# Performance work log

Hardware: AMD Instinct MI355X
Metric: run time of the kernel (lower is better)

The kernel has to match this reference:

```python
import jax, jax.numpy as jnp
import numpy as np

HIDDEN = 1280
NUM_HEADS = 16
HEAD_DIM = HIDDEN // NUM_HEADS  # 80
ROPE_DIM = HEAD_DIM // 2        # 40
THETA = 10000.0
SEQ = 3072


def setup_inputs() -> dict:
    key = jax.random.key(0)
    ks = jax.random.split(key, 6)
    hidden_states = jax.random.normal(ks[0], (SEQ, HIDDEN), dtype=jnp.float32)
    position_ids = jax.random.randint(ks[1], (SEQ, 2), 0, 64, dtype=jnp.int32)
    qkv_w = jax.random.normal(ks[2], (HIDDEN, 3 * HIDDEN), dtype=jnp.float32) * (HIDDEN ** -0.5)
    qkv_b = jax.random.normal(ks[3], (3 * HIDDEN,), dtype=jnp.float32) * 0.02
    o_w = jax.random.normal(ks[4], (HIDDEN, HIDDEN), dtype=jnp.float32) * (HIDDEN ** -0.5)
    o_b = jax.random.normal(ks[5], (HIDDEN,), dtype=jnp.float32) * 0.02
    return {"hidden_states": hidden_states, "position_ids": position_ids,
            "qkv_w": qkv_w, "qkv_b": qkv_b, "o_w": o_w, "o_b": o_b}


def _rotate_half(x):
    x1, x2 = jnp.split(x, 2, axis=-1)
    return jnp.concatenate([-x2, x1], axis=-1)


def reference(hidden_states, position_ids, qkv_w, qkv_b, o_w, o_b):
    seq_len = hidden_states.shape[0]
    # fused QKV projection
    qkv = hidden_states @ qkv_w + qkv_b                     # (S, 3*H*D)
    qkv = qkv.reshape(seq_len, 3, NUM_HEADS, HEAD_DIM)
    q, k, v = qkv[:, 0], qkv[:, 1], qkv[:, 2]               # each (S, h, d)
    # 2D RoPE: inv_freq over rope dim = head_dim // 2
    inv_freq = 1.0 / (THETA ** (jnp.arange(0, ROPE_DIM, 2, dtype=jnp.float32) / ROPE_DIM))
    pos = position_ids.astype(jnp.float32)
    h_freqs = jnp.outer(pos[:, 0], inv_freq)                # (S, rope/2)
    w_freqs = jnp.outer(pos[:, 1], inv_freq)                # (S, rope/2)
    freqs = jnp.concatenate([h_freqs, w_freqs], axis=-1)    # (S, rope)
    emb = jnp.concatenate([freqs, freqs], axis=-1)          # (S, head_dim)
    cos = jnp.cos(emb)[:, None, :]                          # (S, 1, d)
    sin = jnp.sin(emb)[:, None, :]
    q = q * cos + _rotate_half(q) * sin
    k = k * cos + _rotate_half(k) * sin
    # manual attention
    scaling = HEAD_DIM ** -0.5
    attn = jnp.einsum('qhd,khd->hqk', q * scaling, k)       # (h, S, S)
    attn = jax.nn.softmax(attn, axis=-1)
    out = jnp.einsum('hqk,khd->qhd', attn, v)               # (S, h, d)
    out = out.reshape(seq_len, HIDDEN)
    return out @ o_w + o_b
```

## Files before the change

### kernel.cpp

```cpp
#include <hip/hip_runtime.h>

#define SEQ  3072
#define HID  1280
#define NH   16
#define HD   80
#define NQKV 3840
#define KSP  2

typedef unsigned short u16;
typedef unsigned int u32;
typedef __attribute__((ext_vector_type(8))) short short8;
typedef __attribute__((ext_vector_type(4))) short short4v;
typedef __attribute__((ext_vector_type(4))) float floatx4;

__device__ __forceinline__ u16 f2bf(float x) {
    u32 u = __float_as_uint(x);
    u += 0x7fffu + ((u >> 16) & 1u);
    return (u16)(u >> 16);
}
__device__ __forceinline__ u32 packrne(float a, float b) {
    return (u32)f2bf(a) | ((u32)f2bf(b) << 16);
}

typedef const __attribute__((address_space(1))) unsigned int* gp1_t;
typedef __attribute__((address_space(3))) unsigned int* lp3_t;
__device__ __forceinline__ void gld16(const void* g, void* l) {
    __builtin_amdgcn_global_load_lds((gp1_t)g, (lp3_t)l, 16, 0, 0);
}

__device__ __forceinline__ int swz80(int c, int r) {
    return (c < 8) ? (c ^ (r & 7)) : (8 + ((c - 8) ^ ((r >> 2) & 1)));
}

__global__ void prep_k(const int* __restrict__ pos, float* __restrict__ cosb,
                       float* __restrict__ sinb, const float* __restrict__ hs,
                       u16* __restrict__ hH, const float* __restrict__ qkvw,
                       u16* __restrict__ wT, const float* __restrict__ ow,
                       u16* __restrict__ owT) {
    __shared__ float tile[32][33];
    const int b = blockIdx.x, t = threadIdx.x;
    if (b < 480) {
        int i = b * 256 + t;
        int s = i / 40, j = i % 40;
        float p = (float)((j < 20) ? pos[s * 2] : pos[s * 2 + 1]);
        int k = (j < 20) ? j : j - 20;
        float inv = powf(10000.0f, -(float)k / 20.0f);
        float a = p * inv;
        cosb[s * 40 + j] = cosf(a);
        sinb[s * 40 + j] = sinf(a);
    } else if (b < 4320) {
        int i = (b - 480) * 256 + t;
        const float4 x = ((const float4*)hs)[i];
        uint2 o;
        o.x = packrne(x.x, x.y);
        o.y = packrne(x.z, x.w);
        ((uint2*)hH)[i] = o;
    } else {
        const float* w;
        u16* dst;
        int K, N, nx, ky;
        if (b < 9120) {
            int i = b - 4320;
            nx = i % 120; ky = i / 120; w = qkvw; dst = wT; K = HID; N = NQKV;
        } else {
            int i = b - 9120;
            nx = i % 40; ky = i / 40; w = ow; dst = owT; K = HID; N = HID;
        }
        int n0 = nx * 32, k0 = ky * 32;
        int c = t & 31, r8 = t >> 5;
        for (int rr = r8; rr < 32; rr += 8)
            tile[rr][c] = w[(size_t)(k0 + rr) * N + n0 + c];
        __syncthreads();
        for (int rr = r8; rr < 32; rr += 8)
            dst[(size_t)(n0 + rr) * K + k0 + c] = f2bf(tile[c][rr]);
    }
}

__global__ __launch_bounds__(256, 3) void gemm_bf16_k(
    const u16* __restrict__ A, const u16* __restrict__ B,
    const float* __restrict__ bias, float* __restrict__ C,
    int M, int N, int K, int mode) {
    __shared__ u16 lA[128 * 64], lB[128 * 64];
    const int t = threadIdx.x, lane = t & 63, w = t >> 6;
    const int qi = lane & 15, quad = lane >> 4;
    int id = blockIdx.x;
    int xcd = id & 7, sN = id >> 3;
    int m_idx, n_idx;
    if (mode == 0) {
        n_idx = (xcd & 1) * 15 + sN % 15;
        m_idx = (xcd >> 1) * 6 + sN / 15;
    } else {
        m_idx = xcd * 3 + sN / 10;
        n_idx = sN % 10;
    }
    const int m0 = m_idx * 128, n0 = n_idx * 128;
    const int wm = (w >> 1) * 64, wn = (w & 1) * 64;

    floatx4 acc[4][4];
    for (int mi = 0; mi < 4; mi++)
        for (int ni = 0; ni < 4; ni++) acc[mi][ni] = (floatx4){0.f, 0.f, 0.f, 0.f};

    const int rg = lane >> 3;
    const int ce = ((lane & 7) ^ rg) * 8;
    size_t gA[4], gB[4];
    for (int g = 0; g < 4; g++) {
        int row = w * 32 + g * 8 + rg;
        gA[g] = (size_t)(m0 + row) * K + ce;
        gB[g] = (size_t)(n0 + row) * K + ce;
    }

    for (int k0 = 0; k0 < K; k0 += 64) {
        for (int g = 0; g < 4; g++) {
            gld16(A + gA[g] + k0, &lA[(w * 32 + g * 8) * 64]);
            gld16(B + gB[g] + k0, &lB[(w * 32 + g * 8) * 64]);
        }
        __syncthreads();
        short8 af[4][2], bf[4][2];
        for (int mi = 0; mi < 4; mi++) {
            int row = wm + mi * 16 + qi;
            for (int kh = 0; kh < 2; kh++)
                af[mi][kh] = *(const short8*)&lA[row * 64 + (((kh * 4 + quad) ^ (row & 7)) << 3)];
        }
        for (int ni = 0; ni < 4; ni++) {
            int row = wn + ni * 16 + qi;
            for (int kh = 0; kh < 2; kh++)
                bf[ni][kh] = *(const short8*)&lB[row * 64 + (((kh * 4 + quad) ^ (row & 7)) << 3)];
        }
        for (int mi = 0; mi < 4; mi++)
            for (int ni = 0; ni < 4; ni++) {
                acc[mi][ni] = __builtin_amdgcn_mfma_f32_16x16x32_bf16(af[mi][0], bf[ni][0], acc[mi][ni], 0, 0, 0);
                acc[mi][ni] = __builtin_amdgcn_mfma_f32_16x16x32_bf16(af[mi][1], bf[ni][1], acc[mi][ni], 0, 0, 0);
            }
        __syncthreads();
    }
    for (int mi = 0; mi < 4; mi++)
        for (int ni = 0; ni < 4; ni++) {
            int col = n0 + wn + ni * 16 + qi;
            int rowb = m0 + wm + mi * 16 + quad * 4;
            float b = bias[col];
            for (int r = 0; r < 4; r++)
                C[(size_t)(rowb + r) * N + col] = acc[mi][ni][r] + b;
        }
}

__global__ void pack_qkv_k(const float* __restrict__ qkv, const float* __restrict__ cosb,
                           const float* __restrict__ sinb,
                           u16* __restrict__ Qs, u16* __restrict__ Ks, u16* __restrict__ Vs) {
    __shared__ float lv[80 * 65];
    const int t = threadIdx.x;
    const int h = blockIdx.y, s0 = blockIdx.x * 64;
    const float qsc = 0.11180339887498949f * 1.4426950408889634f;

    for (int i = t; i < 64 * 10; i += 256) {
        int rl = i / 10, jg = i % 10;
        int s = s0 + rl, j = jg * 4;
        const float4 cc = *(const float4*)&cosb[s * 40 + j];
        const float4 ss = *(const float4*)&sinb[s * 40 + j];
        const float* qb = qkv + (size_t)s * NQKV + h * HD;
        const float4 q1 = *(const float4*)&qb[j];
        const float4 q2 = *(const float4*)&qb[j + 40];
        const float* kb = qb + HID;
        const float4 k1 = *(const float4*)&kb[j];
        const float4 k2 = *(const float4*)&kb[j + 40];
        uint2 qo1, qo2, ko1, ko2;
        qo1.x = packrne((q1.x * cc.x - q2.x * ss.x) * qsc, (q1.y * cc.y - q2.y * ss.y) * qsc);
        qo1.y = packrne((q1.z * cc.z - q2.z * ss.z) * qsc, (q1.w * cc.w - q2.w * ss.w) * qsc);
        qo2.x = packrne((q2.x * cc.x + q1.x * ss.x) * qsc, (q2.y * cc.y + q1.y * ss.y) * qsc);
        qo2.y = packrne((q2.z * cc.z + q1.z * ss.z) * qsc, (q2.w * cc.w + q1.w * ss.w) * qsc);
        ko1.x = packrne(k1.x * cc.x - k2.x * ss.x, k1.y * cc.y - k2.y * ss.y);
        ko1.y = packrne(k1.z * cc.z - k2.z * ss.z, k1.w * cc.w - k2.w * ss.w);
        ko2.x = packrne(k2.x * cc.x + k1.x * ss.x, k2.y * cc.y + k1.y * ss.y);
        ko2.y = packrne(k2.z * cc.z + k1.z * ss.z, k2.w * cc.w + k1.w * ss.w);
        size_t base = (size_t)(h * SEQ + s) * 80;
        int sub0 = j & 7, sub1 = (j + 40) & 7;
        int p0 = swz80(j >> 3, s);
        int p1 = swz80((j + 40) >> 3, s);
        *(uint2*)&Qs[base + p0 * 8 + sub0] = qo1;
        *(uint2*)&Qs[base + p1 * 8 + sub1] = qo2;
        *(uint2*)&Ks[base + p0 * 8 + sub0] = ko1;
        *(uint2*)&Ks[base + p1 * 8 + sub1] = ko2;
    }
    for (int i = t; i < 64 * 80; i += 256) {
        int rl = i / 80, d = i % 80;
        lv[d * 65 + rl] = qkv[(size_t)(s0 + rl) * NQKV + 2 * HID + h * HD + d];
    }
    __syncthreads();
    for (int i = t; i < 80 * 16; i += 256) {
        int d = i / 16, g = i % 16;
        int c2l = g * 4;
        float v0 = lv[d * 65 + c2l], v1 = lv[d * 65 + c2l + 1];
        float v2 = lv[d * 65 + c2l + 2], v3 = lv[d * 65 + c2l + 3];
        int pc = (g >> 1) ^ (d & 7);
        uint2 o;
        o.x = packrne(v0, v1);
        o.y = packrne(v2, v3);
        *(uint2*)&Vs[((size_t)h * HD + d) * SEQ + s0 + pc * 8 + (g & 1) * 4] = o;
    }
}

__global__ __launch_bounds__(256, 3) void attn_k(
    const u16* __restrict__ Qs, const u16* __restrict__ Ks, const u16* __restrict__ Vs,
    float* __restrict__ Op, float* __restrict__ lp) {
    __shared__ u16 kbuf[2][5120];
    __shared__ u16 vbuf[2][5120];
    __shared__ u16 pls[4][1024];

    const int t = threadIdx.x, lane = t & 63, w = t >> 6;
    const int qi = lane & 15, quad = lane >> 4;
    const int h = blockIdx.y, q0 = blockIdx.x * 128, ksp = blockIdx.z;
    const int kc0 = ksp * (SEQ / 2);
    u16* const kflat = &kbuf[0][0];

    {
        const u16* Qt = Qs + (size_t)(h * SEQ + q0) * 80;
        for (int j = 0; j < 5; j++) {
            int o = (w * 5 + j) * 512;
            gld16(Qt + o + lane * 8, kflat + o);
        }
    }
    __syncthreads();
    short8 bq[2][3];
    for (int qg = 0; qg < 2; qg++) {
        const u16* rb = &kflat[(w * 32 + qg * 16 + qi) * 80];
        bq[qg][0] = *(const short8*)&rb[(quad ^ (qi & 7)) << 3];
        bq[qg][1] = *(const short8*)&rb[((4 + quad) ^ (qi & 7)) << 3];
        short4v t2 = *(const short4v*)&rb[((8 + ((quad >> 1) ^ ((qi >> 2) & 1))) << 3) + ((quad & 1) << 2)];
        bq[qg][2] = (short8){t2.x, t2.y, t2.z, t2.w, 0, 0, 0, 0};
    }
    __syncthreads();

    float l_lane[2] = {0.f, 0.f};
    floatx4 acco[2][5];
    for (int qg = 0; qg < 2; qg++)
        for (int dt = 0; dt < 5; dt++) acco[qg][dt] = (floatx4){0.f, 0.f, 0.f, 0.f};

    auto stage = [&](int it, int buf) {
        int kc = kc0 + it * 64;
        const u16* Kt = Ks + (size_t)(h * SEQ + kc) * 80;
        for (int i = w; i < 10; i += 4)
            gld16(Kt + i * 512 + lane * 8, &kbuf[buf][i * 512]);
        const u16* Vt = Vs + (size_t)h * HD * SEQ + kc;
        for (int i = w; i < 10; i += 4) {
            int p16 = i * 64 + lane;
            int d = p16 >> 3, pc = p16 & 7;
            gld16(Vt + (size_t)d * SEQ + pc * 8, &vbuf[buf][i * 512]);
        }
    };
    stage(0, 0);
    __syncthreads();

    const int NT = (SEQ / 2) / 64;
    char* const myp = (char*)&pls[w][0];
    for (int it = 0; it < NT; it++) {
        int cur = it & 1;
        if (it + 1 < NT) stage(it + 1, cur ^ 1);
        const u16* kb = &kbuf[cur][0];
        const u16* vb = &vbuf[cur][0];
        for (int c2 = 0; c2 < 2; c2++) {
            for (int ktl = 0; ktl < 2; ktl++) {
                int arow = (c2 * 2 + ktl) * 16 + qi;
                const u16* rb = &kb[arow * 80];
                short8 a0 = *(const short8*)&rb[(quad ^ (qi & 7)) << 3];
                short8 a1 = *(const short8*)&rb[((4 + quad) ^ (qi & 7)) << 3];
                short4v a2v = *(const short4v*)&rb[((8 + ((quad >> 1) ^ ((qi >> 2) & 1))) << 3) + ((quad & 1) << 2)];
                short8 a2 = (short8){a2v.x, a2v.y, a2v.z, a2v.w, 0, 0, 0, 0};
                for (int qg = 0; qg < 2; qg++) {
                    floatx4 s = (floatx4){0.f, 0.f, 0.f, 0.f};
                    s = __builtin_amdgcn_mfma_f32_16x16x32_bf16(a0, bq[qg][0], s, 0, 0, 0);
                    s = __builtin_amdgcn_mfma_f32_16x16x32_bf16(a1, bq[qg][1], s, 0, 0, 0);
                    s = __builtin_amdgcn_mfma_f32_16x16x32_bf16(a2, bq[qg][2], s, 0, 0, 0);
                    float e0 = __builtin_amdgcn_exp2f(s[0]);
                    float e1 = __builtin_amdgcn_exp2f(s[1]);
                    float e2 = __builtin_amdgcn_exp2f(s[2]);
                    float e3 = __builtin_amdgcn_exp2f(s[3]);
                    l_lane[qg] += (e0 + e1) + (e2 + e3);
                    uint2 pk;
                    pk.x = __builtin_amdgcn_perm(__float_as_uint(e1), __float_as_uint(e0), 0x07060302u);
                    pk.y = __builtin_amdgcn_perm(__float_as_uint(e3), __float_as_uint(e2), 0x07060302u);
                    int chunk = qg * 4 + 2 * ktl + (quad >> 1);
                    *(uint2*)(myp + qi * 128 + ((chunk ^ (qi & 7)) << 4) + ((quad & 1) << 3)) = pk;
                }
            }
            short8 bp0 = *(const short8*)(myp + qi * 128 + (((quad) ^ (qi & 7)) << 4));
            short8 bp1 = *(const short8*)(myp + qi * 128 + (((4 + quad) ^ (qi & 7)) << 4));
            int pv = (4 * c2 + quad) ^ (qi & 7);
            for (int dt = 0; dt < 5; dt++) {
                short8 av = *(const short8*)&vb[((dt * 16 + qi) * 8 + pv) * 8];
                acco[0][dt] = __builtin_amdgcn_mfma_f32_16x16x32_bf16(av, bp0, acco[0][dt], 0, 0, 0);
                acco[1][dt] = __builtin_amdgcn_mfma_f32_16x16x32_bf16(av, bp1, acco[1][dt], 0, 0, 0);
            }
        }
        __syncthreads();
    }

    for (int qg = 0; qg < 2; qg++) {
        float lq = l_lane[qg];
        lq += __shfl_xor(lq, 16);
        lq += __shfl_xor(lq, 32);
        int q = q0 + w * 32 + qg * 16 + qi;
        if (quad == 0) lp[(size_t)(ksp * NH + h) * SEQ + q] = lq;
        for (int dt = 0; dt < 5; dt++)
            for (int r = 0; r < 4; r++) {
                int d = dt * 16 + quad * 4 + r;
                Op[((size_t)(ksp * NH + h) * HD + d) * SEQ + q] = acco[qg][dt][r];
            }
    }
}

__global__ void merge_k(const float* __restrict__ Op, const float* __restrict__ lp,
                        u16* __restrict__ att) {
    __shared__ float ls[HD * 65];
    __shared__ float li[64];
    const int t = threadIdx.x;
    const int h = blockIdx.y, q0 = blockIdx.x * 64;
    for (int i = t; i < HD * 16; i += 256) {
        int d = i / 16, g = i % 16;
        size_t a0 = ((size_t)h * HD + d) * SEQ + q0 + g * 4;
        size_t a1 = ((size_t)(NH + h) * HD + d) * SEQ + q0 + g * 4;
        const float4 v0 = *(const float4*)&Op[a0];
        const float4 v1 = *(const float4*)&Op[a1];
        ls[d * 65 + g * 4 + 0] = v0.x + v1.x;
        ls[d * 65 + g * 4 + 1] = v0.y + v1.y;
        ls[d * 65 + g * 4 + 2] = v0.z + v1.z;
        ls[d * 65 + g * 4 + 3] = v0.w + v1.w;
    }
    if (t < 64)
        li[t] = 1.0f / (lp[(size_t)h * SEQ + q0 + t] + lp[(size_t)(NH + h) * SEQ + q0 + t]);
    __syncthreads();
    for (int i = t; i < 64 * 40; i += 256) {
        int ql = i / 40, dg = i % 40;
        int d0 = dg * 2;
        float s = li[ql];
        u32 o = packrne(ls[d0 * 65 + ql] * s, ls[(d0 + 1) * 65 + ql] * s);
        *(u32*)&att[(size_t)(q0 + ql) * HID + h * HD + d0] = o;
    }
}

extern "C" void kernel_launch(void* const* d_in, const int* in_sizes, int n_in,
                              void* d_out, int out_size, void* d_ws, size_t ws_size,
                              hipStream_t stream) {
    const float* hs   = (const float*)d_in[0];
    const int*   pos  = (const int*)d_in[1];
    const float* qkvw = (const float*)d_in[2];
    const float* qkvb = (const float*)d_in[3];
    const float* ow   = (const float*)d_in[4];
    const float* ob   = (const float*)d_in[5];
    float* out = (float*)d_out;

    char* p = (char*)d_ws;
    auto alloc = [&](size_t bytes) {
        char* r = p;
        p += (bytes + 255) & ~(size_t)255;
        return r;
    };
    float* cosb = (float*)alloc((size_t)SEQ * 40 * 4);
    float* sinb = (float*)alloc((size_t)SEQ * 40 * 4);
    u16* owT = (u16*)alloc((size_t)HID * HID * 2);
    char* pool1 = alloc(7864320 + 9830400);
    u16* hH = (u16*)pool1;
    u16* wT = (u16*)(pool1 + 7864320);
    u16* Qs = (u16*)pool1;
    u16* Ks = (u16*)(pool1 + 7864320);
    char* pool2 = alloc((size_t)SEQ * NQKV * 4);
    float* qkv_s = (float*)pool2;
    u16* att  = (u16*)pool2;
    float* Op = (float*)(pool2 + 7864320);
    float* lp = (float*)(pool2 + 39321600);
    u16* Vs = (u16*)alloc((size_t)NH * HD * SEQ * 2);

    hipLaunchKernelGGL(prep_k, dim3(10720), dim3(256), 0, stream,
                       pos, cosb, sinb, hs, hH, qkvw, wT, ow, owT);
    hipLaunchKernelGGL(gemm_bf16_k, dim3(720), dim3(256), 0, stream,
                       hH, wT, qkvb, qkv_s, SEQ, NQKV, HID, 0);
    hipLaunchKernelGGL(pack_qkv_k, dim3(SEQ / 64, NH), dim3(256), 0, stream,
                       qkv_s, cosb, sinb, Qs, Ks, Vs);
    hipLaunchKernelGGL(attn_k, dim3(SEQ / 128, NH, 2), dim3(256), 0, stream,
                       Qs, Ks, Vs, Op, lp);
    hipLaunchKernelGGL(merge_k, dim3(SEQ / 64, NH), dim3(256), 0, stream, Op, lp, att);
    hipLaunchKernelGGL(gemm_bf16_k, dim3(240), dim3(256), 0, stream,
                       att, owT, ob, out, SEQ, HID, HID, 1);
}
```

Baseline: 232.4 us.

## Keep softmax probabilities in registers by permuting V key layout for PV MFMA

Instead of writing exponentiated scores to a per-wave LDS buffer and reading them back as the B operand, the probabilities are packed directly into registers and used as the A operand of the PV MFMA. To make this work, the V transpose kernel reorders keys within each 64-key tile so that V's K-dimension matches the MFMA output row ordering. Output stores become vectorized float4 writes, and dropping the pls shared buffer lets launch bounds raise occupancy to 4 blocks per CU. This adds register pressure and relies on the permuted key ordering being consistent between kernels.

Result: no change. 234.6 us (+0.9%).

```diff
diff --git a/kernel.cpp b/kernel.cpp
--- a/kernel.cpp
+++ b/kernel.cpp
@@ -12,6 +12,7 @@
 typedef __attribute__((ext_vector_type(8))) short short8;
 typedef __attribute__((ext_vector_type(4))) short short4v;
 typedef __attribute__((ext_vector_type(4))) float floatx4;
+typedef __attribute__((ext_vector_type(4))) u32 u32x4;
 
 __device__ __forceinline__ u16 f2bf(float x) {
     u32 u = __float_as_uint(x);
@@ -187,23 +188,23 @@
     __syncthreads();
     for (int i = t; i < 80 * 16; i += 256) {
         int d = i / 16, g = i % 16;
-        int c2l = g * 4;
-        float v0 = lv[d * 65 + c2l], v1 = lv[d * 65 + c2l + 1];
-        float v2 = lv[d * 65 + c2l + 2], v3 = lv[d * 65 + c2l + 3];
-        int pc = (g >> 1) ^ (d & 7);
+        int u = g >> 1, h2 = g & 1;
+        int kbase = ((u >> 2) * 32) + ((u & 3) * 4) + 16 * h2;
+        float v0 = lv[d * 65 + kbase], v1 = lv[d * 65 + kbase + 1];
+        float v2 = lv[d * 65 + kbase + 2], v3 = lv[d * 65 + kbase + 3];
+        int pc = u ^ (d & 7);
         uint2 o;
         o.x = packrne(v0, v1);
         o.y = packrne(v2, v3);
-        *(uint2*)&Vs[((size_t)h * HD + d) * SEQ + s0 + pc * 8 + (g & 1) * 4] = o;
-    }
-}
-
-__global__ __launch_bounds__(256, 3) void attn_k(
+        *(uint2*)&Vs[((size_t)h * HD + d) * SEQ + s0 + pc * 8 + h2 * 4] = o;
+    }
+}
+
+__global__ __launch_bounds__(256, 4) void attn_k(
     const u16* __restrict__ Qs, const u16* __restrict__ Ks, const u16* __restrict__ Vs,
     float* __restrict__ Op, float* __restrict__ lp) {
     __shared__ u16 kbuf[2][5120];
     __shared__ u16 vbuf[2][5120];
-    __shared__ u16 pls[4][1024];
 
     const int t = threadIdx.x, lane = t & 63, w = t >> 6;
     const int qi = lane & 15, quad = lane >> 4;
@@ -250,13 +251,13 @@
     __syncthreads();
 
     const int NT = (SEQ / 2) / 64;
-    char* const myp = (char*)&pls[w][0];
     for (int it = 0; it < NT; it++) {
         int cur = it & 1;
         if (it + 1 < NT) stage(it + 1, cur ^ 1);
         const u16* kb = &kbuf[cur][0];
         const u16* vb = &vbuf[cur][0];
         for (int c2 = 0; c2 < 2; c2++) {
+            u32x4 pka[2];
             for (int ktl = 0; ktl < 2; ktl++) {
                 int arow = (c2 * 2 + ktl) * 16 + qi;
                 const u16* rb = &kb[arow * 80];
@@ -274,20 +275,17 @@
                     float e2 = __builtin_amdgcn_exp2f(s[2]);
                     float e3 = __builtin_amdgcn_exp2f(s[3]);
                     l_lane[qg] += (e0 + e1) + (e2 + e3);
-                    uint2 pk;
-                    pk.x = __builtin_amdgcn_perm(__float_as_uint(e1), __float_as_uint(e0), 0x07060302u);
-                    pk.y = __builtin_amdgcn_perm(__float_as_uint(e3), __float_as_uint(e2), 0x07060302u);
-                    int chunk = qg * 4 + 2 * ktl + (quad >> 1);
-                    *(uint2*)(myp + qi * 128 + ((chunk ^ (qi & 7)) << 4) + ((quad & 1) << 3)) = pk;
+                    pka[qg][2 * ktl] = __builtin_amdgcn_perm(__float_as_uint(e1), __float_as_uint(e0), 0x07060302u);
+                    pka[qg][2 * ktl + 1] = __builtin_amdgcn_perm(__float_as_uint(e3), __float_as_uint(e2), 0x07060302u);
                 }
             }
-            short8 bp0 = *(const short8*)(myp + qi * 128 + (((quad) ^ (qi & 7)) << 4));
-            short8 bp1 = *(const short8*)(myp + qi * 128 + (((4 + quad) ^ (qi & 7)) << 4));
+            short8 ap0 = *(short8*)&pka[0];
+            short8 ap1 = *(short8*)&pka[1];
             int pv = (4 * c2 + quad) ^ (qi & 7);
             for (int dt = 0; dt < 5; dt++) {
-                short8 av = *(const short8*)&vb[((dt * 16 + qi) * 8 + pv) * 8];
-                acco[0][dt] = __builtin_amdgcn_mfma_f32_16x16x32_bf16(av, bp0, acco[0][dt], 0, 0, 0);
-                acco[1][dt] = __builtin_amdgcn_mfma_f32_16x16x32_bf16(av, bp1, acco[1][dt], 0, 0, 0);
+                short8 bv = *(const short8*)&vb[((dt * 16 + qi) * 8 + pv) * 8];
+                acco[0][dt] = __builtin_amdgcn_mfma_f32_16x16x32_bf16(ap0, bv, acco[0][dt], 0, 0, 0);
+                acco[1][dt] = __builtin_amdgcn_mfma_f32_16x16x32_bf16(ap1, bv, acco[1][dt], 0, 0, 0);
             }
         }
         __syncthreads();
@@ -299,11 +297,11 @@
         lq += __shfl_xor(lq, 32);
         int q = q0 + w * 32 + qg * 16 + qi;
         if (quad == 0) lp[(size_t)(ksp * NH + h) * SEQ + q] = lq;
-        for (int dt = 0; dt < 5; dt++)
-            for (int r = 0; r < 4; r++) {
-                int d = dt * 16 + quad * 4 + r;
-                Op[((size_t)(ksp * NH + h) * HD + d) * SEQ + q] = acco[qg][dt][r];
-            }
+        int qrow = q0 + w * 32 + qg * 16 + quad * 4;
+        for (int dt = 0; dt < 5; dt++) {
+            int d = dt * 16 + qi;
+            *(floatx4*)&Op[((size_t)(ksp * NH + h) * HD + d) * SEQ + qrow] = acco[qg][dt];
+        }
     }
 }
 
```
